# Kernel optimization log

Hardware: AMD Instinct MI355X
Metric: run time of the kernel (lower is better)

Reference implementation:

```python
import jax, jax.numpy as jnp
import numpy as np

B, S, H, NH = 4, 2048, 1024, 16
HD = H // NH
EPS = 1e-12

def setup_inputs() -> dict:
    key = jax.random.key(0)
    ks = jax.random.split(key, 8)
    sc = 1.0 / np.sqrt(H)
    return {
        "input_tensor": jax.random.normal(ks[0], (B, S, H), jnp.float32),
        "attention_mask": jnp.zeros((B, 1, 1, S), jnp.float32),
        "Wq": jax.random.normal(ks[1], (H, H), jnp.float32) * sc,
        "bq": jnp.zeros((H,), jnp.float32),
        "Wk": jax.random.normal(ks[2], (H, H), jnp.float32) * sc,
        "bk": jnp.zeros((H,), jnp.float32),
        "Wv": jax.random.normal(ks[3], (H, H), jnp.float32) * sc,
        "bv": jnp.zeros((H,), jnp.float32),
        "Wo": jax.random.normal(ks[4], (H, H), jnp.float32) * sc,
        "bo": jnp.zeros((H,), jnp.float32),
        "ln_w": jnp.ones((H,), jnp.float32),
        "ln_b": jnpp_zeros if False else jnp.zeros((H,), jnp.float32),
    }

def reference(input_tensor, attention_mask, Wq, bq, Wk, bk, Wv, bv, Wo, bo, ln_w, ln_b):
    x = input_tensor  # [B,S,H]
    # QKV projections (torch Linear: x @ W.T + b), split heads -> [B,S,NH,HD]
    q = (x @ Wq.T + bq).reshape(B, S, NH, HD)
    k = (x @ Wk.T + bk).reshape(B, S, NH, HD)
    v = (x @ Wv.T + bv).reshape(B, S, NH, HD)
    # scores [B,NH,S,S]
    scores = jnp.einsum('bqhd,bkhd->bhqk', q, k) / jnp.sqrt(jnp.float32(HD))
    scores = scores + attention_mask  # broadcast [B,1,1,S]
    probs = jax.nn.softmax(scores, axis=-1)  # dropout is identity in eval
    ctx = jnp.einsum('bhqk,bkhd->bqhd', probs, v).reshape(B, S, H)
    # output dense + residual + LayerNorm (TF-style eps inside sqrt)
    h = ctx @ Wo.T + bo + x
    u = h.mean(-1, keepdims=True)
    s = jnp.mean((h - u) ** 2, axis=-1, keepdims=True)
    return ln_w * (h - u) / jnp.sqrt(s + EPS) + ln_b
```

## Files before the change

### kernel.cpp

```cpp
#include <hip/hip_runtime.h>

typedef __bf16 bf16;
typedef __bf16 bf16x8 __attribute__((ext_vector_type(8)));
typedef __bf16 bf16x4 __attribute__((ext_vector_type(4)));
typedef float floatx4 __attribute__((ext_vector_type(4)));
typedef int   intx4  __attribute__((ext_vector_type(4)));
typedef int   intx2  __attribute__((ext_vector_type(2)));

#define MFMA16(a,b,c) __builtin_amdgcn_mfma_f32_16x16x32_bf16((a),(b),(c),0,0,0)

constexpr int Bc  = 4;
constexpr int Sc  = 2048;
constexpr int Hc  = 1024;
constexpr int NHc = 16;
constexpr int HDc = 64;
constexpr int Mc  = Bc * Sc;
constexpr int KIT = Hc / 32;
constexpr float L2E = 1.44269504088896f;

union U64  { bf16x4 h; intx2 i; };

__device__ __forceinline__ void ld16(const bf16* g, bf16* l) {
    __builtin_amdgcn_global_load_lds(
        (const __attribute__((address_space(1))) void*)g,
        (__attribute__((address_space(3))) void*)l, 16, 0, 0);
}

__global__ void detect_k(const unsigned short* __restrict__ x, int* __restrict__ flag)
{
    if (threadIdx.x == 0 && blockIdx.x == 0) {
        float mx = 0.f;
        for (int i = 0; i < 256; ++i) {
            unsigned int bits = ((unsigned int)x[i]) << 16;
            float v = __uint_as_float(bits);
            if (!isfinite(v)) { mx = 1e30f; break; }
            mx = fmaxf(mx, fabsf(v));
        }
        *flag = (mx > 1e6f) ? 1 : 0;
    }
}

__global__ __launch_bounds__(256)
void conv_all_k(const void* __restrict__ x,
                const void* __restrict__ Wq, const void* __restrict__ Wk,
                const void* __restrict__ Wv, const void* __restrict__ Wo,
                const void* __restrict__ mask,
                const void* __restrict__ bq, const void* __restrict__ bk,
                const void* __restrict__ bv, const void* __restrict__ bo,
                const void* __restrict__ lnw, const void* __restrict__ lnb,
                bf16* __restrict__ xb, bf16* __restrict__ wdst,
                float* maskf, float* bqf, float* bkf, float* bvf,
                float* bof, float* lnwf, float* lnbf,
                const int* __restrict__ flag)
{
    const int g = blockIdx.x * 256 + threadIdx.x;
    const int fl = *flag;
    if (g < 1048576) {
        if (fl) {
            const float* s = (const float*)x + (size_t)g * 8;
            union { intx4 v; bf16 e[8]; } o;
#pragma unroll
            for (int j = 0; j < 8; ++j) o.e[j] = (bf16)s[j];
            *(intx4*)(xb + (size_t)g * 8) = o.v;
        } else {
            *(intx4*)(xb + (size_t)g * 8) = *((const intx4*)x + g);
        }
    } else if (g < 1048576 + 524288) {
        const int gw = g - 1048576;
        const int wsel = gw >> 17, go = gw & 131071;
        const void* s = (wsel == 0) ? Wq : (wsel == 1) ? Wk : (wsel == 2) ? Wv : Wo;
        if (fl) {
            const float* sp = (const float*)s + (size_t)go * 8;
            union { intx4 v; bf16 e[8]; } o;
#pragma unroll
            for (int j = 0; j < 8; ++j) o.e[j] = (bf16)sp[j];
            *(intx4*)(wdst + (size_t)gw * 8) = o.v;
        } else {
            *(intx4*)(wdst + (size_t)gw * 8) = *((const intx4*)s + go);
        }
    } else {
        const int gs = g - 1048576 - 524288;
        if (gs >= 1792) return;
        const void* src; float* dst; int off; float scl = 1.0f;
        if (gs < 1024) { src = mask; dst = maskf; off = gs * 8; scl = L2E; }
        else {
            const int a = (gs - 1024) >> 7;
            off = ((gs - 1024) & 127) * 8;
            switch (a) {
                case 0: src = bq;  dst = bqf;  break;
                case 1: src = bk;  dst = bkf;  break;
                case 2: src = bv;  dst = bvf;  break;
                case 3: src = bo;  dst = bof;  break;
                case 4: src = lnw; dst = lnwf; break;
                default: src = lnb; dst = lnbf; break;
            }
        }
        if (fl) {
            const float* s = (const float*)src + off;
#pragma unroll
            for (int j = 0; j < 8; ++j) dst[off + j] = s[j] * scl;
        } else {
            union { intx4 v; bf16 e[8]; } u;
            u.v = *(const intx4*)((const bf16*)src + off);
#pragma unroll
            for (int j = 0; j < 8; ++j) dst[off + j] = (float)u.e[j] * scl;
        }
    }
}

template<int SWAP>
__device__ __forceinline__
void gemm_core(const bf16* __restrict__ A, const bf16* __restrict__ W,
               int m0, int n0, int t, bf16* As, bf16* Bs, floatx4 (&acc)[4][4])
{
    const int l  = t & 63, w = t >> 6;
    const int wr = w >> 1, wc = w & 1;
    const int lq = l >> 4, ln = l & 15;
    const int srow = t >> 2;
    const int scol = (t & 3) * 8;

    const bf16* a0 = A + (size_t)(m0 + srow) * Hc + scol;
    const bf16* b0 = W + (size_t)(n0 + srow) * Hc + scol;
    bf16* lA0 = As + srow * 32 + scol;
    bf16* lA1 = lA0 + 64 * 32;
    bf16* lB0 = Bs + srow * 32 + scol;
    bf16* lB1 = lB0 + 64 * 32;

    for (int kb = 0; kb < KIT; ++kb) {
        const int off = kb * 32;
        ld16(a0 + off,           lA0);
        ld16(a0 + 64 * Hc + off, lA1);
        ld16(b0 + off,           lB0);
        ld16(b0 + 64 * Hc + off, lB1);
        __syncthreads();

        bf16x8 af[4], bw[4];
#pragma unroll
        for (int i = 0; i < 4; ++i)
            af[i] = *(const bf16x8*)&As[(wr * 64 + i * 16 + ln) * 32 + lq * 8];
#pragma unroll
        for (int j = 0; j < 4; ++j)
            bw[j] = *(const bf16x8*)&Bs[(wc * 64 + j * 16 + ln) * 32 + lq * 8];
#pragma unroll
        for (int i = 0; i < 4; ++i)
#pragma unroll
            for (int j = 0; j < 4; ++j)
                acc[i][j] = SWAP ? MFMA16(bw[j], af[i], acc[i][j])
                                 : MFMA16(af[i], bw[j], acc[i][j]);
        __syncthreads();
    }
}

__global__ __launch_bounds__(256)
void qkv_gemm(const bf16* __restrict__ x,
              const bf16* __restrict__ Wq, const float* __restrict__ bq,
              const bf16* __restrict__ Wk, const float* __restrict__ bk,
              const bf16* __restrict__ Wv, const float* __restrict__ bv,
              bf16* __restrict__ qo, bf16* __restrict__ ko, bf16* __restrict__ vto)
{
    __shared__ __align__(16) bf16 smem[8704];
    const int z = blockIdx.z;
    const bf16*  W    = (z == 0) ? Wq : (z == 1) ? Wk : Wv;
    const float* bias = (z == 0) ? bq : (z == 1) ? bk : bv;

    const int m0 = blockIdx.y * 128, n0 = blockIdx.x * 128;
    const int t  = threadIdx.x;
    const int l  = t & 63, w = t >> 6;
    const int wr = w >> 1, wc = w & 1;
    const int lq = l >> 4, ln = l & 15;

    if (z < 2) {
        floatx4 acc[4][4] = {};
        gemm_core<1>(x, W, m0, n0, t, smem, smem + 4096, acc);
        bf16* out = (z == 0) ? qo : ko;
        const float sc = (z == 0) ? 0.125f * L2E : 1.0f;
#pragma unroll
        for (int j = 0; j < 4; ++j) {
            const int feat = n0 + wc * 64 + j * 16 + lq * 4;
            const floatx4 bb = *(const floatx4*)&bias[feat];
            const int hh = feat >> 6, dd = feat & 63;
#pragma unroll
            for (int i = 0; i < 4; ++i) {
                const int xrow = m0 + wr * 64 + i * 16 + ln;
                const int bi = xrow >> 11, si = xrow & (Sc - 1);
                U64 pk;
#pragma unroll
                for (int r = 0; r < 4; ++r) pk.h[r] = (bf16)((acc[i][j][r] + bb[r]) * sc);
                *(intx2*)&out[(((size_t)bi * NHc + hh) * Sc + si) * HDc + dd] = pk.i;
            }
        }
    } else {
        floatx4 acc[4][4] = {};
        gemm_core<0>(x, W, m0, n0, t, smem, smem + 4096, acc);
        bf16* Ct = smem;
        const int bi = m0 >> 11, s0 = m0 & (Sc - 1);
        for (int h2 = 0; h2 < 2; ++h2) {
            __syncthreads();
            if (wc == h2) {
#pragma unroll
                for (int j = 0; j < 4; ++j) {
                    const int c = j * 16 + ln;
                    const float bb = bias[n0 + h2 * 64 + c];
#pragma unroll
                    for (int i = 0; i < 4; ++i) {
                        U64 pk;
#pragma unroll
                        for (int r = 0; r < 4; ++r) pk.h[r] = (bf16)(acc[i][j][r] + bb);
                        *(intx2*)&Ct[c * 136 + wr * 64 + i * 16 + lq * 4] = pk.i;
                    }
                }
            }
            __syncthreads();
#pragma unroll
            for (int u = 0; u < 4; ++u) {
                const int id = t + 256 * u;
                const int c = id >> 4, rg = id & 15;
                const int hh = (n0 >> 6) + h2;
                intx4 val = *(const intx4*)&Ct[c * 136 + rg * 8];
                *(intx4*)&vto[(((size_t)bi * NHc + hh) * HDc + c) * Sc + s0 + rg * 8] = val;
            }
        }
    }
}

__global__ __launch_bounds__(256)
void oproj_gemm(const bf16* __restrict__ ctx, const bf16* __restrict__ Wo,
                const float* __restrict__ bo, const bf16* __restrict__ xb,
                bf16* __restrict__ hout)
{
    __shared__ __align__(16) bf16 smem[8192];
    const int m0 = blockIdx.y * 128, n0 = blockIdx.x * 128;
    const int t  = threadIdx.x;
    floatx4 acc[4][4] = {};
    gemm_core<1>(ctx, Wo, m0, n0, t, smem, smem + 4096, acc);

    const int l  = t & 63, w = t >> 6;
    const int wr = w >> 1, wc = w & 1;
    const int lq = l >> 4, ln = l & 15;
#pragma unroll
    for (int j = 0; j < 4; ++j) {
        const int col = n0 + wc * 64 + j * 16 + lq * 4;
        const floatx4 bb = *(const floatx4*)&bo[col];
#pragma unroll
        for (int i = 0; i < 4; ++i) {
            const int row = m0 + wr * 64 + i * 16 + ln;
            U64 rx;
            rx.i = *(const intx2*)&xb[(size_t)row * Hc + col];
            U64 pk;
#pragma unroll
            for (int r = 0; r < 4; ++r)
                pk.h[r] = (bf16)(acc[i][j][r] + bb[r] + (float)rx.h[r]);
            *(intx2*)&hout[(size_t)row * Hc + col] = pk.i;
        }
    }
}

__global__ __launch_bounds__(256, 2)
void attention(const bf16* __restrict__ q, const bf16* __restrict__ k,
               const bf16* __restrict__ vt, const float* __restrict__ maskf,
               bf16* __restrict__ ctx)
{
    __shared__ __align__(16) bf16 Ks[64][72];
    __shared__ __align__(16) bf16 Vs[64][72];
    __shared__ __align__(16) bf16 Pt[256][72];

    const int idx = blockIdx.x;
    const int qt = idx & 7, h = (idx >> 3) & 15, b = idx >> 7;
    const int bh = b * NHc + h;
    const int t = threadIdx.x, w = t >> 6, l = t & 63;
    const int lq = l >> 4, ln = l & 15;
    const int q0 = qt * 256 + w * 64;

    bf16x8 qf[4][2];
#pragma unroll
    for (int qb = 0; qb < 4; ++qb)
#pragma unroll
        for (int kh = 0; kh < 2; ++kh)
            qf[qb][kh] = *(const bf16x8*)(q + ((size_t)bh * Sc + q0 + qb * 16 + ln) * HDc
                                            + kh * 32 + lq * 8);

    bf16x8 ones8;
#pragma unroll
    for (int j = 0; j < 8; ++j) ones8[j] = (bf16)1.0f;

    floatx4 o[4][4] = {};
    floatx4 accl[4] = {};

    const bf16* kbase = k  + (size_t)bh * Sc * HDc;
    const bf16* vbase = vt + (size_t)bh * HDc * Sc;
    const float* mbase = maskf + b * Sc;

    const int sr = t >> 2, scg = (t & 3) * 16;
    intx4 kr0 = *(const intx4*)(kbase + (size_t)sr * HDc + scg);
    intx4 kr1 = *(const intx4*)(kbase + (size_t)sr * HDc + scg + 8);
    intx4 vr0 = *(const intx4*)(vbase + (size_t)sr * Sc + scg);
    intx4 vr1 = *(const intx4*)(vbase + (size_t)sr * Sc + scg + 8);

    for (int kt = 0; kt < Sc / 64; ++kt) {
        *(intx4*)&Ks[sr][scg]     = kr0;
        *(intx4*)&Ks[sr][scg + 8] = kr1;
        *(intx4*)&Vs[sr][scg]     = vr0;
        *(intx4*)&Vs[sr][scg + 8] = vr1;
        __syncthreads();

        if (kt + 1 < Sc / 64) {
            const int kn = (kt + 1) * 64;
            kr0 = *(const intx4*)(kbase + (size_t)(kn + sr) * HDc + scg);
            kr1 = *(const intx4*)(kbase + (size_t)(kn + sr) * HDc + scg + 8);
            vr0 = *(const intx4*)(vbase + (size_t)sr * Sc + kn + scg);
            vr1 = *(const intx4*)(vbase + (size_t)sr * Sc + kn + scg + 8);
        }

        floatx4 mvl[4];
#pragma unroll
        for (int cb = 0; cb < 4; ++cb)
            mvl[cb] = *(const floatx4*)(mbase + kt * 64 + cb * 16 + lq * 4);

        bf16x8 kf[4][2];
#pragma unroll
        for (int cb = 0; cb < 4; ++cb) {
            kf[cb][0] = *(const bf16x8*)&Ks[cb * 16 + ln][lq * 8];
            kf[cb][1] = *(const bf16x8*)&Ks[cb * 16 + ln][32 + lq * 8];
        }

#pragma unroll
        for (int qb = 0; qb < 4; ++qb) {
#pragma unroll
            for (int cb = 0; cb < 4; ++cb) {
                floatx4 a = mvl[cb];
                a = MFMA16(kf[cb][0], qf[qb][0], a);
                a = MFMA16(kf[cb][1], qf[qb][1], a);
                U64 pk;
#pragma unroll
                for (int r = 0; r < 4; ++r)
                    pk.h[r] = (bf16)__builtin_amdgcn_exp2f(a[r]);
                *(intx2*)&Pt[w * 64 + qb * 16 + ln][cb * 16 + lq * 4] = pk.i;
            }
        }

        bf16x8 vf[4][2];
#pragma unroll
        for (int db = 0; db < 4; ++db) {
            vf[db][0] = *(const bf16x8*)&Vs[db * 16 + ln][lq * 8];
            vf[db][1] = *(const bf16x8*)&Vs[db * 16 + ln][32 + lq * 8];
        }
#pragma unroll
        for (int qb = 0; qb < 4; ++qb) {
            bf16x8 pf0 = *(const bf16x8*)&Pt[w * 64 + qb * 16 + ln][lq * 8];
            bf16x8 pf1 = *(const bf16x8*)&Pt[w * 64 + qb * 16 + ln][32 + lq * 8];
#pragma unroll
            for (int db = 0; db < 4; ++db) {
                o[qb][db] = MFMA16(vf[db][0], pf0, o[qb][db]);
                o[qb][db] = MFMA16(vf[db][1], pf1, o[qb][db]);
            }
            accl[qb] = MFMA16(ones8, pf0, accl[qb]);
            accl[qb] = MFMA16(ones8, pf1, accl[qb]);
        }
        __syncthreads();
    }

#pragma unroll
    for (int qb = 0; qb < 4; ++qb) {
        const float li = 1.f / accl[qb][0];
        const int qg = q0 + qb * 16 + ln;
#pragma unroll
        for (int db = 0; db < 4; ++db) {
            U64 pk;
#pragma unroll
            for (int r = 0; r < 4; ++r) pk.h[r] = (bf16)(o[qb][db][r] * li);
            *(intx2*)&ctx[((size_t)b * Sc + qg) * Hc + h * HDc + db * 16 + lq * 4] = pk.i;
        }
    }
}

__global__ __launch_bounds__(256)
void layernorm_k(const bf16* __restrict__ hbuf, const float* __restrict__ lw,
                 const float* __restrict__ lb, void* __restrict__ outp,
                 const int* __restrict__ flag)
{
    const int row = blockIdx.x;
    const int t = threadIdx.x;
    const bf16* hp = hbuf + (size_t)row * Hc;

    union { intx2 i2; bf16 e[4]; } pk;
    pk.i2 = *(const intx2*)(hp + t * 4);
    float v[4], sum = 0.f, sq = 0.f;
#pragma unroll
    for (int i = 0; i < 4; ++i) {
        v[i] = (float)pk.e[i];
        sum += v[i];
        sq  += v[i] * v[i];
    }
#pragma unroll
    for (int off = 1; off < 64; off <<= 1) {
        sum += __shfl_xor(sum, off, 64);
        sq  += __shfl_xor(sq,  off, 64);
    }
    __shared__ float ssum[4], ssq[4];
    const int w = t >> 6;
    if ((t & 63) == 0) { ssum[w] = sum; ssq[w] = sq; }
    __syncthreads();
    sum = ssum[0] + ssum[1] + ssum[2] + ssum[3];
    sq  = ssq[0]  + ssq[1]  + ssq[2]  + ssq[3];

    const float mean = sum * (1.f / (float)Hc);
    const float var  = sq * (1.f / (float)Hc) - mean * mean;
    const float rstd = rsqrtf(var + 1e-12f);

    float ov[4];
#pragma unroll
    for (int i = 0; i < 4; ++i) {
        const int c = t * 4 + i;
        ov[i] = lw[c] * (v[i] - mean) * rstd + lb[c];
    }
    if (*flag) {
        float* of = (float*)outp + (size_t)row * Hc + t * 4;
#pragma unroll
        for (int i = 0; i < 4; ++i) of[i] = ov[i];
    } else {
        union { intx2 i2; bf16 e[4]; } po;
#pragma unroll
        for (int i = 0; i < 4; ++i) po.e[i] = (bf16)ov[i];
        *(intx2*)((bf16*)outp + (size_t)row * Hc + t * 4) = po.i2;
    }
}

extern "C" void kernel_launch(void* const* d_in, const int* in_sizes, int n_in,
                              void* d_out, int out_size, void* d_ws, size_t ws_size,
                              hipStream_t stream)
{
    const void* x    = d_in[0];
    const void* mask = d_in[1];
    const void* Wq   = d_in[2];
    const void* bq   = d_in[3];
    const void* Wk   = d_in[4];
    const void* bk   = d_in[5];
    const void* Wv   = d_in[6];
    const void* bv   = d_in[7];
    const void* Wo   = d_in[8];
    const void* bo   = d_in[9];
    const void* lnw  = d_in[10];
    const void* lnb  = d_in[11];

    char* ws = (char*)d_ws;
    const size_t MB = 1024 * 1024;
    int*   flag  = (int*)ws;
    float* maskf = (float*)(ws + 4096);
    float* bqf   = (float*)(ws + 64 * 1024);
    float* bkf   = bqf + Hc;
    float* bvf   = bkf + Hc;
    float* bof   = bvf + Hc;
    float* lnwf  = bof + Hc;
    float* lnbf  = lnwf + Hc;
    bf16* xb  = (bf16*)(ws + 1 * MB);
    bf16* wqb = (bf16*)(ws + 17 * MB);
    bf16* wkb = (bf16*)(ws + 19 * MB);
    bf16* wvb = (bf16*)(ws + 21 * MB);
    bf16* wob = (bf16*)(ws + 23 * MB);
    bf16* qb  = (bf16*)(ws + 25 * MB);
    bf16* kb  = (bf16*)(ws + 41 * MB);
    bf16* vtb = (bf16*)(ws + 57 * MB);
    bf16* cb  = (bf16*)(ws + 73 * MB);
    bf16* hb  = qb;

    detect_k<<<1, 64, 0, stream>>>((const unsigned short*)x, flag);

    conv_all_k<<<6153, 256, 0, stream>>>(x, Wq, Wk, Wv, Wo, mask,
                                         bq, bk, bv, bo, lnw, lnb,
                                         xb, wqb, maskf, bqf, bkf, bvf,
                                         bof, lnwf, lnbf, flag);

    dim3 gqkv(Hc / 128, Mc / 128, 3);
    qkv_gemm<<<gqkv, 256, 0, stream>>>(xb, wqb, bqf, wkb, bkf, wvb, bvf, qb, kb, vtb);
    attention<<<dim3(Bc * NHc * (Sc / 256)), 256, 0, stream>>>(qb, kb, vtb, maskf, cb);
    oproj_gemm<<<dim3(Hc / 128, Mc / 128), 256, 0, stream>>>(cb, wob, bof, xb, hb);
    layernorm_k<<<dim3(Mc), 256, 0, stream>>>(hb, lnwf, lnbf, d_out, flag);
}
```

Measured before the change: 322.4 us.

## Restructure attention with async LDS double-buffering, register-resident P, and XCD-aware block mapping

The attention kernel now stages K/V tiles into a swizzled, double-buffered LDS layout using direct global-to-LDS loads, prefetching the next tile while the current one is computed. This replaces register staging and removes one barrier per iteration. Probabilities no longer round-trip through LDS: they are rearranged into MFMA operand layout with permlane swap instructions, and the row sums come from VALU adds plus a final shuffle rather than extra ones-vector MFMAs. Blocks are remapped so each XCD works on a contiguous group of heads for L2 locality, and s_setprio raises priority around the MFMA section. The gain depends on the swizzle and permlane layouts being correct, and the new code adds register pressure.

```diff
diff --git a/kernel.cpp b/kernel.cpp
--- a/kernel.cpp
+++ b/kernel.cpp
@@ -260,17 +260,26 @@
                const bf16* __restrict__ vt, const float* __restrict__ maskf,
                bf16* __restrict__ ctx)
 {
-    __shared__ __align__(16) bf16 Ks[64][72];
-    __shared__ __align__(16) bf16 Vs[64][72];
-    __shared__ __align__(16) bf16 Pt[256][72];
-
-    const int idx = blockIdx.x;
-    const int qt = idx & 7, h = (idx >> 3) & 15, b = idx >> 7;
-    const int bh = b * NHc + h;
+    __shared__ __align__(16) bf16 KV[2][2][64][64];
+
+    const int raw = blockIdx.x;
+    const int xcd = raw & 7, jj = raw >> 3;
+    const int bh  = xcd * 8 + (jj >> 3);
+    const int qt  = jj & 7;
+    const int b = bh >> 4, h = bh & 15;
     const int t = threadIdx.x, w = t >> 6, l = t & 63;
     const int lq = l >> 4, ln = l & 15;
     const int q0 = qt * 256 + w * 64;
 
+    const bf16* kg = k  + (size_t)bh * Sc * HDc;
+    const bf16* vg = vt + (size_t)bh * HDc * Sc;
+    const float* mbase = maskf + b * Sc;
+
+    const int rr  = l >> 3;
+    const int gsw = ((l & 7) ^ rr) << 3;
+    const int r0  = w * 16 + rr, r1 = r0 + 8;
+    const int dco = (l & 7) << 3;
+
     bf16x8 qf[4][2];
 #pragma unroll
     for (int qb = 0; qb < 4; ++qb)
@@ -279,89 +288,112 @@
             qf[qb][kh] = *(const bf16x8*)(q + ((size_t)bh * Sc + q0 + qb * 16 + ln) * HDc
                                             + kh * 32 + lq * 8);
 
-    bf16x8 ones8;
-#pragma unroll
-    for (int j = 0; j < 8; ++j) ones8[j] = (bf16)1.0f;
-
     floatx4 o[4][4] = {};
-    floatx4 accl[4] = {};
-
-    const bf16* kbase = k  + (size_t)bh * Sc * HDc;
-    const bf16* vbase = vt + (size_t)bh * HDc * Sc;
-    const float* mbase = maskf + b * Sc;
-
-    const int sr = t >> 2, scg = (t & 3) * 16;
-    intx4 kr0 = *(const intx4*)(kbase + (size_t)sr * HDc + scg);
-    intx4 kr1 = *(const intx4*)(kbase + (size_t)sr * HDc + scg + 8);
-    intx4 vr0 = *(const intx4*)(vbase + (size_t)sr * Sc + scg);
-    intx4 vr1 = *(const intx4*)(vbase + (size_t)sr * Sc + scg + 8);
+    float dacc[4] = {0.f, 0.f, 0.f, 0.f};
+
+    auto stage = [&](int buf, int kt) {
+        bf16* Kd = &KV[buf][0][0][0];
+        bf16* Vd = &KV[buf][1][0][0];
+        ld16(kg + (size_t)(kt * 64 + r0) * HDc + gsw, Kd + r0 * 64 + dco);
+        ld16(kg + (size_t)(kt * 64 + r1) * HDc + gsw, Kd + r1 * 64 + dco);
+        ld16(vg + (size_t)r0 * Sc + kt * 64 + gsw,    Vd + r0 * 64 + dco);
+        ld16(vg + (size_t)r1 * Sc + kt * 64 + gsw,    Vd + r1 * 64 + dco);
+    };
+
+    stage(0, 0);
+    int cur = 0;
 
     for (int kt = 0; kt < Sc / 64; ++kt) {
-        *(intx4*)&Ks[sr][scg]     = kr0;
-        *(intx4*)&Ks[sr][scg + 8] = kr1;
-        *(intx4*)&Vs[sr][scg]     = vr0;
-        *(intx4*)&Vs[sr][scg + 8] = vr1;
         __syncthreads();
-
-        if (kt + 1 < Sc / 64) {
-            const int kn = (kt + 1) * 64;
-            kr0 = *(const intx4*)(kbase + (size_t)(kn + sr) * HDc + scg);
-            kr1 = *(const intx4*)(kbase + (size_t)(kn + sr) * HDc + scg + 8);
-            vr0 = *(const intx4*)(vbase + (size_t)sr * Sc + kn + scg);
-            vr1 = *(const intx4*)(vbase + (size_t)sr * Sc + kn + scg + 8);
-        }
+        if (kt + 1 < Sc / 64) stage(cur ^ 1, kt + 1);
+
+        const bf16* Kb = &KV[cur][0][0][0];
+        const bf16* Vb = &KV[cur][1][0][0];
 
         floatx4 mvl[4];
 #pragma unroll
         for (int cb = 0; cb < 4; ++cb)
             mvl[cb] = *(const floatx4*)(mbase + kt * 64 + cb * 16 + lq * 4);
 
-        bf16x8 kf[4][2];
+        bf16x8 kf[4][2], vf[4][2];
+        const int sw = ln & 7;
 #pragma unroll
         for (int cb = 0; cb < 4; ++cb) {
-            kf[cb][0] = *(const bf16x8*)&Ks[cb * 16 + ln][lq * 8];
-            kf[cb][1] = *(const bf16x8*)&Ks[cb * 16 + ln][32 + lq * 8];
-        }
-
+            const int row = (cb * 16 + ln) * 64;
+#pragma unroll
+            for (int kh = 0; kh < 2; ++kh) {
+                const int cc = ((kh * 4 + lq) ^ sw) << 3;
+                kf[cb][kh] = *(const bf16x8*)&Kb[row + cc];
+                vf[cb][kh] = *(const bf16x8*)&Vb[row + cc];
+            }
+        }
+
+        __builtin_amdgcn_s_setprio(1);
 #pragma unroll
         for (int qb = 0; qb < 4; ++qb) {
+            floatx4 s[4];
 #pragma unroll
             for (int cb = 0; cb < 4; ++cb) {
-                floatx4 a = mvl[cb];
-                a = MFMA16(kf[cb][0], qf[qb][0], a);
-                a = MFMA16(kf[cb][1], qf[qb][1], a);
-                U64 pk;
-#pragma unroll
-                for (int r = 0; r < 4; ++r)
-                    pk.h[r] = (bf16)__builtin_amdgcn_exp2f(a[r]);
-                *(intx2*)&Pt[w * 64 + qb * 16 + ln][cb * 16 + lq * 4] = pk.i;
-            }
-        }
-
-        bf16x8 vf[4][2];
-#pragma unroll
-        for (int db = 0; db < 4; ++db) {
-            vf[db][0] = *(const bf16x8*)&Vs[db * 16 + ln][lq * 8];
-            vf[db][1] = *(const bf16x8*)&Vs[db * 16 + ln][32 + lq * 8];
-        }
-#pragma unroll
-        for (int qb = 0; qb < 4; ++qb) {
-            bf16x8 pf0 = *(const bf16x8*)&Pt[w * 64 + qb * 16 + ln][lq * 8];
-            bf16x8 pf1 = *(const bf16x8*)&Pt[w * 64 + qb * 16 + ln][32 + lq * 8];
+                s[cb] = mvl[cb];
+                s[cb] = MFMA16(kf[cb][0], qf[qb][0], s[cb]);
+                s[cb] = MFMA16(kf[cb][1], qf[qb][1], s[cb]);
+            }
+            unsigned int D[4][2];
+            float ds = 0.f;
+#pragma unroll
+            for (int cb = 0; cb < 4; ++cb)
+#pragma unroll
+                for (int i = 0; i < 2; ++i) {
+                    const float e0 = __builtin_amdgcn_exp2f(s[cb][2 * i]);
+                    const float e1 = __builtin_amdgcn_exp2f(s[cb][2 * i + 1]);
+                    ds += e0 + e1;
+                    union { unsigned int u; bf16 e[2]; } pk2;
+                    pk2.e[0] = (bf16)e0; pk2.e[1] = (bf16)e1;
+                    D[cb][i] = pk2.u;
+                }
+            dacc[qb] += ds;
+
+            unsigned int F0[4], F1[4];
+            {
+                unsigned int A, B;
+                A = D[0][0]; B = D[1][0];
+                asm("v_permlane32_swap_b32 %0, %1" : "+v"(A), "+v"(B));
+                asm("v_permlane16_swap_b32 %0, %1" : "+v"(A), "+v"(B));
+                F0[0] = A; F0[2] = B;
+                A = D[0][1]; B = D[1][1];
+                asm("v_permlane32_swap_b32 %0, %1" : "+v"(A), "+v"(B));
+                asm("v_permlane16_swap_b32 %0, %1" : "+v"(A), "+v"(B));
+                F0[1] = A; F0[3] = B;
+                A = D[2][0]; B = D[3][0];
+                asm("v_permlane32_swap_b32 %0, %1" : "+v"(A), "+v"(B));
+                asm("v_permlane16_swap_b32 %0, %1" : "+v"(A), "+v"(B));
+                F1[0] = A; F1[2] = B;
+                A = D[2][1]; B = D[3][1];
+                asm("v_permlane32_swap_b32 %0, %1" : "+v"(A), "+v"(B));
+                asm("v_permlane16_swap_b32 %0, %1" : "+v"(A), "+v"(B));
+                F1[1] = A; F1[3] = B;
+            }
+            union { unsigned int u[4]; bf16x8 v; } P0, P1;
+#pragma unroll
+            for (int d = 0; d < 4; ++d) { P0.u[d] = F0[d]; P1.u[d] = F1[d]; }
+            const bf16x8 pf0 = P0.v, pf1 = P1.v;
+
 #pragma unroll
             for (int db = 0; db < 4; ++db) {
                 o[qb][db] = MFMA16(vf[db][0], pf0, o[qb][db]);
                 o[qb][db] = MFMA16(vf[db][1], pf1, o[qb][db]);
             }
-            accl[qb] = MFMA16(ones8, pf0, accl[qb]);
-            accl[qb] = MFMA16(ones8, pf1, accl[qb]);
-        }
-        __syncthreads();
+        }
+        __builtin_amdgcn_s_setprio(0);
+        cur ^= 1;
     }
 
 #pragma unroll
     for (int qb = 0; qb < 4; ++qb) {
-        const float li = 1.f / accl[qb][0];
+        float dsum = dacc[qb];
+        dsum += __shfl_xor(dsum, 16, 64);
+        dsum += __shfl_xor(dsum, 32, 64);
+        const float li = 1.f / dsum;
         const int qg = q0 + qb * 16 + ln;
 #pragma unroll
         for (int db = 0; db < 4; ++db) {
```

After: 342.6 us. +6.3%, slower.
